# Kernel optimization log

Measured on AMD Instinct MI355X. Metric: run time of the kernel, lower is better.

## Reference

```python
import jax, jax.numpy as jnp
import numpy as np

N = 100000   # nodes of ntype 'gene'
E = 800000   # edges per metapath
D = 256      # input_dim == output_dim
H = 4        # attn heads
C = D // H   # out_channels per head
M = 2        # num metapaths (tail relations = M + 1, last = self)


def _lrelu(x):
    return jnp.where(x >= 0, x, 0.2 * x)


def _segment_softmax(logits, seg, num_segments):
    # logits: [E, H], seg: [E] int targets
    mx = jax.ops.segment_max(logits, seg, num_segments=num_segments)
    mx = jnp.where(jnp.isfinite(mx), mx, 0.0)  # empty segments -> 0
    ex = jnp.exp(logits - mx[seg])
    den = jax.ops.segment_sum(ex, seg, num_segments=num_segments)
    return ex / (den[seg] + 1e-16)


def setup_inputs() -> dict:
    key = jax.random.key(0)
    ks = jax.random.split(key, 10)
    s = 1.0 / np.sqrt(D)
    return {
        "x": jax.random.normal(ks[0], (N, D), dtype=jnp.float32),
        "edge_index0": jax.random.randint(ks[1], (2, E), 0, N, dtype=jnp.int32),
        "edge_index1": jax.random.randint(ks[2], (2, E), 0, N, dtype=jnp.int32),
        "W_l": jax.random.normal(ks[3], (D, D), dtype=jnp.float32) * s,
        "b_l": jnp.zeros((D,), dtype=jnp.float32),
        "W_r": jax.random.normal(ks[4], (D, D), dtype=jnp.float32) * s,
        "b_r": jnp.zeros((D,), dtype=jnp.float32),
        "attn": jax.random.normal(ks[5], (M, H, 2 * C), dtype=jnp.float32) * (1.0 / np.sqrt(2 * C)),
        "rel_attn_l": jax.random.normal(ks[6], (H, C), dtype=jnp.float32) * (1.0 / np.sqrt(C)),
        "rel_attn_r": jax.random.normal(ks[7], (H, C), dtype=jnp.float32) * (1.0 / np.sqrt(C)),
    }


def reference(x, edge_index0, edge_index1, W_l, b_l, W_r, b_r, attn, rel_attn_l, rel_attn_r):
    # projections -> [N, H, C]  (eval mode: dropout/batchnorm off)
    l = (x @ W_l.T + b_l).reshape(N, H, C)
    r = (x @ W_r.T + b_r).reshape(N, H, C)

    # attn split: first C for x_i (target, r-proj), last C for x_j (source, l-proj);
    # leaky_relu is elementwise so the concat+dot separates exactly.
    def agg(edge_index, m_idx):
        src, tgt = edge_index[0], edge_index[1]
        a_i = jnp.einsum('ehc,hc->eh', _lrelu(r[tgt]), attn[m_idx, :, :C])
        a_j = jnp.einsum('ehc,hc->eh', _lrelu(l[src]), attn[m_idx, :, C:])
        alpha = _segment_softmax(a_i + a_j, tgt, N)          # [E, H]
        msg = l[src] * alpha[:, :, None]                      # [E, H, C]
        return jax.ops.segment_sum(msg, tgt, num_segments=N)  # [N, H, C]

    out0 = agg(edge_index0, 0)
    out1 = agg(edge_index1, 1)
    emb = jnp.stack([out0, out1, r], axis=1)                  # [N, M+1, H, C]

    # relation-level beta attention (get_beta_weights)
    alpha_l = jnp.einsum('nhc,hc->nh', r, rel_attn_l)         # [N, H]
    alpha_r = jnp.einsum('nrhc,hc->nrh', emb, rel_attn_r)     # [N, M+1, H]
    beta = jax.nn.softmax(_lrelu(alpha_l[:, None, :] + alpha_r), axis=1)

    h = (emb * beta[..., None]).sum(axis=1).reshape(N, D)
    return jax.nn.relu(h)
```

## Files before the change

kernel.cpp:

```cpp
#include <hip/hip_runtime.h>
#include <hip/hip_bf16.h>
#include <math.h>

#define D_ 256
#define H_ 4
#define C_ 64

typedef __attribute__((ext_vector_type(8))) short short8;
typedef __attribute__((ext_vector_type(4))) float f32x4;

__device__ inline float lrelu(float v) { return v >= 0.f ? v : 0.2f * v; }

__device__ inline unsigned short f2b(float f) {
    unsigned u = __float_as_uint(f);
    u = (u + 0x7FFFu + ((u >> 16) & 1u)) >> 16;
    return (unsigned short)u;
}
__device__ inline float b2f(unsigned short u) {
    return __uint_as_float(((unsigned)u) << 16);
}

#define GLDS(src, dst) __builtin_amdgcn_global_load_lds(                      \
    (const __attribute__((address_space(1))) void*)(src),                     \
    (__attribute__((address_space(3))) void*)(dst), 16, 0, 0)

__global__ __launch_bounds__(256) void convert_w(
    const float* __restrict__ Wl, const float* __restrict__ Wr,
    unsigned short* __restrict__ Wb)
{
    int i4 = blockIdx.x * 256 + threadIdx.x;
    float4 v = (i4 < 16384) ? ((const float4*)Wl)[i4]
                            : ((const float4*)Wr)[i4 - 16384];
    ushort4 u;
    u.x = f2b(v.x); u.y = f2b(v.y); u.z = f2b(v.z); u.w = f2b(v.w);
    ((ushort4*)Wb)[i4] = u;
}

__device__ __forceinline__ void stage_a(const float* __restrict__ x, float* dst,
                                        int bm, int k0, int wv, int lane, int Mrows)
{
#pragma unroll
    for (int p = 0; p < 4; p++) {
        int ci = (p * 4 + wv) * 64 + lane;
        int row = ci >> 3, cc = ci & 7;
        int gr = bm + row; if (gr >= Mrows) gr = Mrows - 1;
        const float* src = x + (size_t)gr * 256 + k0 + ((cc ^ (row & 7)) << 2);
        GLDS(src, (char*)dst + (size_t)(p * 4 + wv) * 1024);
    }
}
__device__ __forceinline__ void stage_b(const unsigned short* __restrict__ W,
                                        unsigned short* dst, int bn, int k0,
                                        int wv, int lane)
{
#pragma unroll
    for (int p = 0; p < 2; p++) {
        int ci = (p * 4 + wv) * 64 + lane;
        int col = ci >> 2, cc = ci & 3;
        const unsigned short* src = W + (size_t)(bn + col) * 256 + k0 +
                                    ((cc ^ (col & 3)) << 3);
        GLDS(src, (char*)dst + (size_t)(p * 4 + wv) * 1024);
    }
}

template <bool RB16>
__global__ __launch_bounds__(256) void gemm_fused(
    const float* __restrict__ x, const unsigned short* __restrict__ Wb,
    const float* __restrict__ b_l, const float* __restrict__ b_r,
    unsigned short* __restrict__ lout, void* __restrict__ rout,
    int Mrows, int nblk)
{
    int hw = blockIdx.x;
    int orig = hw;
    if ((nblk & 7) == 0) {
        int cpx = nblk >> 3;
        orig = (hw & 7) * cpx + (hw >> 3);
    }
    const int sel = (orig & 3) >> 1;
    const int bn = (orig & 1) * 128;
    const int bm = (orig >> 2) * 128;

    __shared__ float As[2][128 * 32];
    __shared__ unsigned short Bs[2][128 * 32];
    const int tid = threadIdx.x;
    const int lane = tid & 63, wv = tid >> 6;
    const int wr = wv >> 1, wc = wv & 1;
    const unsigned short* W = Wb + (size_t)sel * 65536;

    f32x4 acc[4][4];
#pragma unroll
    for (int m = 0; m < 4; m++)
#pragma unroll
        for (int n = 0; n < 4; n++) acc[m][n] = (f32x4)0.f;

    stage_a(x, As[0], bm, 0, wv, lane, Mrows);
    stage_b(W, Bs[0], bn, 0, wv, lane);
    __syncthreads();

    int cur = 0;
#pragma unroll
    for (int t = 0; t < 8; t++) {
        if (t < 7) {
            stage_a(x, As[cur ^ 1], bm, (t + 1) * 32, wv, lane, Mrows);
            stage_b(W, Bs[cur ^ 1], bn, (t + 1) * 32, wv, lane);
        }
        short8 bfr[4];
#pragma unroll
        for (int n = 0; n < 4; n++) {
            int col = wc * 64 + n * 16 + (lane & 15);
            int sc = (lane >> 4) ^ (col & 3);
            bfr[n] = *(const short8*)&Bs[cur][col * 32 + sc * 8];
        }
        short8 afr[4];
#pragma unroll
        for (int m = 0; m < 4; m++) {
            int row = wr * 64 + m * 16 + (lane & 15);
            int c0 = (lane >> 4) * 2;
            const float* ap = &As[cur][row * 32];
            float4 f0 = *(const float4*)&ap[(c0 ^ (row & 7)) << 2];
            float4 f1 = *(const float4*)&ap[((c0 + 1) ^ (row & 7)) << 2];
            union { short8 v; __hip_bfloat162 b2[4]; } u;
            u.b2[0] = __float22bfloat162_rn(make_float2(f0.x, f0.y));
            u.b2[1] = __float22bfloat162_rn(make_float2(f0.z, f0.w));
            u.b2[2] = __float22bfloat162_rn(make_float2(f1.x, f1.y));
            u.b2[3] = __float22bfloat162_rn(make_float2(f1.z, f1.w));
            afr[m] = u.v;
        }
#pragma unroll
        for (int m = 0; m < 4; m++)
#pragma unroll
            for (int n = 0; n < 4; n++)
                acc[m][n] = __builtin_amdgcn_mfma_f32_16x16x32_bf16(
                    afr[m], bfr[n], acc[m][n], 0, 0, 0);
        __syncthreads();
        cur ^= 1;
    }

    const float* bias = sel ? b_r : b_l;
#pragma unroll
    for (int m = 0; m < 4; m++) {
        int grow0 = bm + wr * 64 + m * 16 + (lane >> 4) * 4;
#pragma unroll
        for (int n = 0; n < 4; n++) {
            int gcol = bn + wc * 64 + n * 16 + (lane & 15);
            float bv = bias[gcol];
#pragma unroll
            for (int q = 0; q < 4; q++) {
                int grow = grow0 + q;
                if (grow < Mrows) {
                    float v = acc[m][n][q] + bv;
                    if (sel == 0) {
                        lout[(size_t)grow * 256 + gcol] = f2b(v);
                    } else {
                        if (RB16) ((unsigned short*)rout)[(size_t)grow * 256 + gcol] = f2b(v);
                        else      ((float*)rout)[(size_t)grow * 256 + gcol] = v;
                    }
                }
            }
        }
    }
}

template <bool RB16>
__global__ __launch_bounds__(256) void node_logits(
    const unsigned short* __restrict__ l, const void* __restrict__ rv,
    const float* __restrict__ attn, const float* __restrict__ rel_l,
    const float* __restrict__ rel_r,
    float2* __restrict__ ej2, float* __restrict__ al, float* __restrict__ rd,
    int Nn)
{
    int lane = threadIdx.x & 63;
    int n = blockIdx.x * 4 + (threadIdx.x >> 6);
    if (n >= Nn) return;
    int h = lane >> 4, q = lane & 15;

    ushort4 lv4 = *(const ushort4*)&l[(size_t)n * D_ + lane * 4];
    float rf[4];
    if (RB16) {
        ushort4 ru = ((const ushort4*)rv)[(size_t)n * 64 + lane];
        rf[0] = b2f(ru.x); rf[1] = b2f(ru.y); rf[2] = b2f(ru.z); rf[3] = b2f(ru.w);
    } else {
        float4 rv4 = ((const float4*)rv)[(size_t)n * 64 + lane];
        rf[0] = rv4.x; rf[1] = rv4.y; rf[2] = rv4.z; rf[3] = rv4.w;
    }
    float4 a0 = *(const float4*)&attn[(0 * H_ + h) * 128 + 64 + q * 4];
    float4 a1 = *(const float4*)&attn[(1 * H_ + h) * 128 + 64 + q * 4];
    float4 wl = *(const float4*)&rel_l[h * C_ + q * 4];
    float4 wr = *(const float4*)&rel_r[h * C_ + q * 4];

    float lf[4] = { b2f(lv4.x), b2f(lv4.y), b2f(lv4.z), b2f(lv4.w) };
    float af0[4] = { a0.x, a0.y, a0.z, a0.w };
    float af1[4] = { a1.x, a1.y, a1.z, a1.w };
    float wlf[4] = { wl.x, wl.y, wl.z, wl.w };
    float wrf[4] = { wr.x, wr.y, wr.z, wr.w };

    float v2 = 0.f, v3 = 0.f, v4 = 0.f, v5 = 0.f, v6 = 0.f;
#pragma unroll
    for (int k = 0; k < 4; k++) {
        float ll = lrelu(lf[k]);
        v2 = fmaf(ll, af0[k], v2);
        v3 = fmaf(ll, af1[k], v3);
        v4 = fmaf(rf[k], wlf[k], v4);
        v5 = fmaf(lf[k], wrf[k], v5);
        v6 = fmaf(rf[k], wrf[k], v6);
    }
#pragma unroll
    for (int off = 1; off < 16; off <<= 1) {
        v2 += __shfl_xor(v2, off);
        v3 += __shfl_xor(v3, off);
        v4 += __shfl_xor(v4, off);
        v5 += __shfl_xor(v5, off);
        v6 += __shfl_xor(v6, off);
    }
    if (q == 0) {
        int NH = Nn * H_;
        int nh = n * H_ + h;
        float e0 = __expf(v2), e1 = __expf(v3);
        ej2[nh]      = make_float2(e0, e0 * v5);
        ej2[NH + nh] = make_float2(e1, e1 * v5);
        al[nh] = v4;
        rd[nh] = v6;
    }
}

__global__ __launch_bounds__(256) void edge_hist(
    const int* __restrict__ ei0, const int* __restrict__ ei1,
    int* __restrict__ hist, int E_, int Nn)
{
    int e = blockIdx.x * 256 + threadIdx.x;
    if (e >= E_) return;
    atomicAdd(&hist[ei0[E_ + e]], 1);
    atomicAdd(&hist[Nn + ei1[E_ + e]], 1);
}

__global__ __launch_bounds__(256) void scan_a(
    const int* __restrict__ hist, int* __restrict__ segoff,
    int* __restrict__ bsum, int Nn)
{
    int m = blockIdx.y;
    int gid = blockIdx.x * 256 + threadIdx.x;
    int lane = threadIdx.x & 63, wid = threadIdx.x >> 6;
    int v = (gid < Nn) ? hist[m * Nn + gid] : 0;
    int incl = v;
#pragma unroll
    for (int off = 1; off < 64; off <<= 1) {
        int u = __shfl_up(incl, off);
        if (lane >= off) incl += u;
    }
    __shared__ int ws[4], wo[4];
    if (lane == 63) ws[wid] = incl;
    __syncthreads();
    if (threadIdx.x == 0) {
        int run = 0;
#pragma unroll
        for (int i = 0; i < 4; i++) { wo[i] = run; run += ws[i]; }
        bsum[m * 512 + blockIdx.x] = run;
    }
    __syncthreads();
    if (gid < Nn) segoff[m * Nn + gid] = incl - v + wo[wid];
}

__global__ __launch_bounds__(512) void scan_b(int* __restrict__ bsum, int nb)
{
    int m = blockIdx.x;
    int* b = bsum + m * 512;
    int tid = threadIdx.x, lane = tid & 63, wid = tid >> 6;
    int v = (tid < nb) ? b[tid] : 0;
    int incl = v;
#pragma unroll
    for (int off = 1; off < 64; off <<= 1) {
        int u = __shfl_up(incl, off);
        if (lane >= off) incl += u;
    }
    __shared__ int ws[8], wo[8];
    if (lane == 63) ws[wid] = incl;
    __syncthreads();
    if (tid == 0) {
        int run = 0;
#pragma unroll
        for (int i = 0; i < 8; i++) { wo[i] = run; run += ws[i]; }
    }
    __syncthreads();
    if (tid < nb) b[tid] = incl - v + wo[wid];
}

__global__ __launch_bounds__(256) void edge_scatter(
    const int* __restrict__ ei0, const int* __restrict__ ei1,
    const int* __restrict__ segoff, const int* __restrict__ bsum,
    int* __restrict__ cursor, int* __restrict__ srcs, int E_, int Nn)
{
    int e = blockIdx.x * 256 + threadIdx.x;
    if (e >= E_) return;
    int t0 = ei0[E_ + e];
    int p0 = segoff[t0] + bsum[t0 >> 8] + atomicAdd(&cursor[t0], 1);
    srcs[p0] = ei0[e];
    int t1 = ei1[E_ + e];
    int p1 = segoff[Nn + t1] + bsum[512 + (t1 >> 8)] + atomicAdd(&cursor[Nn + t1], 1);
    srcs[E_ + p1] = ei1[e];
}

template <bool RB16>
__global__ __launch_bounds__(256) void aggregate(
    const int* __restrict__ hist, const int* __restrict__ segoff,
    const int* __restrict__ bsum,
    const int* __restrict__ srcs, const float2* __restrict__ ej2,
    const float* __restrict__ al, const float* __restrict__ rd,
    const void* __restrict__ rv, const unsigned short* __restrict__ l,
    float* __restrict__ out, int Nn, int E_)
{
    int lane = threadIdx.x & 63;
    int t = blockIdx.x * 4 + (threadIdx.x >> 6);
    if (t >= Nn) return;
    int h = lane >> 4;
    int NH = Nn * H_;
    int nh = t * H_ + h;

    float4 rrow;
    if (RB16) {
        ushort4 ru = ((const ushort4*)rv)[(size_t)t * 64 + lane];
        rrow = make_float4(b2f(ru.x), b2f(ru.y), b2f(ru.z), b2f(ru.w));
    } else {
        rrow = ((const float4*)rv)[(size_t)t * 64 + lane];
    }
    float a = al[nh];
    float rdv = rd[nh];

    int beg0 = segoff[t]      + bsum[t >> 8],         deg0 = hist[t];
    int beg1 = segoff[Nn + t] + bsum[512 + (t >> 8)], deg1 = hist[Nn + t];

    float4 acc0 = make_float4(0.f, 0.f, 0.f, 0.f);
    float4 acc1 = make_float4(0.f, 0.f, 0.f, 0.f);
    float den0 = 0.f, pn0 = 0.f, den1 = 0.f, pn1 = 0.f;

#pragma unroll 4
    for (int j = 0; j < deg0; j++) {
        int s = srcs[beg0 + j];
        float2 v = ej2[(size_t)s * H_ + h];
        den0 += v.x; pn0 += v.y;
        ushort4 lv = *(const ushort4*)&l[(size_t)s * D_ + lane * 4];
        acc0.x = fmaf(b2f(lv.x), v.x, acc0.x);
        acc0.y = fmaf(b2f(lv.y), v.x, acc0.y);
        acc0.z = fmaf(b2f(lv.z), v.x, acc0.z);
        acc0.w = fmaf(b2f(lv.w), v.x, acc0.w);
    }
    const float2* ep1 = ej2 + NH;
#pragma unroll 4
    for (int j = 0; j < deg1; j++) {
        int s = srcs[E_ + beg1 + j];
        float2 v = ep1[(size_t)s * H_ + h];
        den1 += v.x; pn1 += v.y;
        ushort4 lv = *(const ushort4*)&l[(size_t)s * D_ + lane * 4];
        acc1.x = fmaf(b2f(lv.x), v.x, acc1.x);
        acc1.y = fmaf(b2f(lv.y), v.x, acc1.y);
        acc1.z = fmaf(b2f(lv.z), v.x, acc1.z);
        acc1.w = fmaf(b2f(lv.w), v.x, acc1.w);
    }

    float b0 = lrelu(a + pn0 / (den0 + 1e-16f));
    float b1 = lrelu(a + pn1 / (den1 + 1e-16f));
    float b2 = lrelu(a + rdv);
    float mm = fmaxf(b0, fmaxf(b1, b2));
    float e0 = __expf(b0 - mm), e1 = __expf(b1 - mm), e2 = __expf(b2 - mm);
    float inv = 1.f / (e0 + e1 + e2);
    float wm0 = e0 * inv / (den0 + 1e-16f);
    float wm1 = e1 * inv / (den1 + 1e-16f);
    float b2v = e2 * inv;

    float4 o;
    o.x = fmaxf(fmaf(wm0, acc0.x, fmaf(wm1, acc1.x, b2v * rrow.x)), 0.f);
    o.y = fmaxf(fmaf(wm0, acc0.y, fmaf(wm1, acc1.y, b2v * rrow.y)), 0.f);
    o.z = fmaxf(fmaf(wm0, acc0.z, fmaf(wm1, acc1.z, b2v * rrow.z)), 0.f);
    o.w = fmaxf(fmaf(wm0, acc0.w, fmaf(wm1, acc1.w, b2v * rrow.w)), 0.f);
    *(float4*)&out[(size_t)t * D_ + lane * 4] = o;
}

extern "C" void kernel_launch(void* const* d_in, const int* in_sizes, int n_in,
                              void* d_out, int out_size, void* d_ws, size_t ws_size,
                              hipStream_t stream) {
    const float* x     = (const float*)d_in[0];
    const int*   ei0   = (const int*)d_in[1];
    const int*   ei1   = (const int*)d_in[2];
    const float* W_l   = (const float*)d_in[3];
    const float* b_l   = (const float*)d_in[4];
    const float* W_r   = (const float*)d_in[5];
    const float* b_r   = (const float*)d_in[6];
    const float* attn  = (const float*)d_in[7];
    const float* rel_l = (const float*)d_in[8];
    const float* rel_r = (const float*)d_in[9];
    float* out = (float*)d_out;

    const int Nn = in_sizes[0] / D_;
    const int E_ = in_sizes[1] / 2;
    const size_t ND = (size_t)Nn * D_;
    const int NH = Nn * H_;

    char* base = (char*)d_ws;
    unsigned short* l = (unsigned short*)base;      size_t off = ND * 2;
    float2* ej2  = (float2*)(base + off); off += (size_t)2 * NH * 8;
    float* al    = (float*)(base + off);  off += (size_t)NH * 4;
    float* rd    = (float*)(base + off);  off += (size_t)NH * 4;
    int* hist    = (int*)(base + off);    off += (size_t)2 * Nn * 4;
    int* cursor  = (int*)(base + off);    off += (size_t)2 * Nn * 4;
    int* segoff  = (int*)(base + off);    off += (size_t)2 * Nn * 4;
    int* bsum    = (int*)(base + off);    off += (size_t)1024 * 4;
    int* srcs    = (int*)(base + off);    off += (size_t)2 * E_ * 4;
    unsigned short* Wb = (unsigned short*)(base + off); off += (size_t)2 * 65536 * 2;
    unsigned short* rb = (unsigned short*)(base + off);
    const bool rb16 = (ws_size >= off + ND * 2);
    void* r_any = rb16 ? (void*)rb : (void*)out;

    hipMemsetAsync(hist, 0, (size_t)4 * Nn * 4, stream);

    convert_w<<<128, 256, 0, stream>>>(W_l, W_r, Wb);

    int rowTiles = (Nn + 127) / 128;
    int nblk = 4 * rowTiles;
    if (rb16)
        gemm_fused<true ><<<nblk, 256, 0, stream>>>(x, Wb, b_l, b_r, l, r_any, Nn, nblk);
    else
        gemm_fused<false><<<nblk, 256, 0, stream>>>(x, Wb, b_l, b_r, l, r_any, Nn, nblk);

    if (rb16)
        node_logits<true ><<<(Nn + 3) / 4, 256, 0, stream>>>(
            l, r_any, attn, rel_l, rel_r, ej2, al, rd, Nn);
    else
        node_logits<false><<<(Nn + 3) / 4, 256, 0, stream>>>(
            l, r_any, attn, rel_l, rel_r, ej2, al, rd, Nn);

    int eb = (E_ + 255) / 256;
    int nb = (Nn + 255) / 256;
    edge_hist<<<eb, 256, 0, stream>>>(ei0, ei1, hist, E_, Nn);
    scan_a<<<dim3(nb, 2), 256, 0, stream>>>(hist, segoff, bsum, Nn);
    scan_b<<<2, 512, 0, stream>>>(bsum, nb);
    edge_scatter<<<eb, 256, 0, stream>>>(ei0, ei1, segoff, bsum, cursor, srcs, E_, Nn);

    if (rb16)
        aggregate<true ><<<(Nn + 3) / 4, 256, 0, stream>>>(
            hist, segoff, bsum, srcs, ej2, al, rd, r_any, l, out, Nn, E_);
    else
        aggregate<false><<<(Nn + 3) / 4, 256, 0, stream>>>(
            hist, segoff, bsum, srcs, ej2, al, rd, r_any, l, out, Nn, E_);
}
```

Measured before the change: 446.7 us.

## Fuse node logits into GEMM epilogue and split aggregation across metapath waves

```diff
diff --git a/kernel.cpp b/kernel.cpp
--- a/kernel.cpp
+++ b/kernel.cpp
@@ -66,7 +66,10 @@
 __global__ __launch_bounds__(256) void gemm_fused(
     const float* __restrict__ x, const unsigned short* __restrict__ Wb,
     const float* __restrict__ b_l, const float* __restrict__ b_r,
+    const float* __restrict__ attn, const float* __restrict__ rel_l,
+    const float* __restrict__ rel_r,
     unsigned short* __restrict__ lout, void* __restrict__ rout,
+    float2* __restrict__ ej2, float* __restrict__ al, float* __restrict__ rd,
     int Mrows, int nblk)
 {
     int hw = blockIdx.x;
@@ -136,89 +139,71 @@
     }
 
     const float* bias = sel ? b_r : b_l;
+    const int NH = Mrows * H_;
+    const int h = (bn >> 6) + wc;
+    float bv[4], w0[4], w1[4], w2[4];
+    int gcol[4];
+#pragma unroll
+    for (int n = 0; n < 4; n++) {
+        int c = n * 16 + (lane & 15);
+        gcol[n] = bn + wc * 64 + c - (wc * 64 + c) + wc * 64 + c;
+        gcol[n] = bn + wc * 64 + c;
+        bv[n] = bias[gcol[n]];
+        if (sel == 0) {
+            w0[n] = attn[(0 * H_ + h) * 128 + 64 + c];
+            w1[n] = attn[(1 * H_ + h) * 128 + 64 + c];
+            w2[n] = rel_r[h * C_ + c];
+        } else {
+            w0[n] = rel_l[h * C_ + c];
+            w1[n] = rel_r[h * C_ + c];
+        }
+    }
 #pragma unroll
     for (int m = 0; m < 4; m++) {
-        int grow0 = bm + wr * 64 + m * 16 + (lane >> 4) * 4;
-#pragma unroll
-        for (int n = 0; n < 4; n++) {
-            int gcol = bn + wc * 64 + n * 16 + (lane & 15);
-            float bv = bias[gcol];
-#pragma unroll
-            for (int q = 0; q < 4; q++) {
-                int grow = grow0 + q;
-                if (grow < Mrows) {
-                    float v = acc[m][n][q] + bv;
+#pragma unroll
+        for (int q = 0; q < 4; q++) {
+            int grow = bm + wr * 64 + m * 16 + (lane >> 4) * 4 + q;
+            bool ok = grow < Mrows;
+            float p0 = 0.f, p1 = 0.f, p2 = 0.f;
+#pragma unroll
+            for (int n = 0; n < 4; n++) {
+                float v = acc[m][n][q] + bv[n];
+                if (ok) {
                     if (sel == 0) {
-                        lout[(size_t)grow * 256 + gcol] = f2b(v);
+                        lout[(size_t)grow * 256 + gcol[n]] = f2b(v);
                     } else {
-                        if (RB16) ((unsigned short*)rout)[(size_t)grow * 256 + gcol] = f2b(v);
-                        else      ((float*)rout)[(size_t)grow * 256 + gcol] = v;
+                        if (RB16) ((unsigned short*)rout)[(size_t)grow * 256 + gcol[n]] = f2b(v);
+                        else      ((float*)rout)[(size_t)grow * 256 + gcol[n]] = v;
                     }
                 }
+                if (sel == 0) {
+                    float lr = lrelu(v);
+                    p0 = fmaf(lr, w0[n], p0);
+                    p1 = fmaf(lr, w1[n], p1);
+                    p2 = fmaf(v, w2[n], p2);
+                } else {
+                    p0 = fmaf(v, w0[n], p0);
+                    p1 = fmaf(v, w1[n], p1);
+                }
             }
-        }
-    }
-}
-
-template <bool RB16>
-__global__ __launch_bounds__(256) void node_logits(
-    const unsigned short* __restrict__ l, const void* __restrict__ rv,
-    const float* __restrict__ attn, const float* __restrict__ rel_l,
-    const float* __restrict__ rel_r,
-    float2* __restrict__ ej2, float* __restrict__ al, float* __restrict__ rd,
-    int Nn)
-{
-    int lane = threadIdx.x & 63;
-    int n = blockIdx.x * 4 + (threadIdx.x >> 6);
-    if (n >= Nn) return;
-    int h = lane >> 4, q = lane & 15;
-
-    ushort4 lv4 = *(const ushort4*)&l[(size_t)n * D_ + lane * 4];
-    float rf[4];
-    if (RB16) {
-        ushort4 ru = ((const ushort4*)rv)[(size_t)n * 64 + lane];
-        rf[0] = b2f(ru.x); rf[1] = b2f(ru.y); rf[2] = b2f(ru.z); rf[3] = b2f(ru.w);
-    } else {
-        float4 rv4 = ((const float4*)rv)[(size_t)n * 64 + lane];
-        rf[0] = rv4.x; rf[1] = rv4.y; rf[2] = rv4.z; rf[3] = rv4.w;
-    }
-    float4 a0 = *(const float4*)&attn[(0 * H_ + h) * 128 + 64 + q * 4];
-    float4 a1 = *(const float4*)&attn[(1 * H_ + h) * 128 + 64 + q * 4];
-    float4 wl = *(const float4*)&rel_l[h * C_ + q * 4];
-    float4 wr = *(const float4*)&rel_r[h * C_ + q * 4];
-
-    float lf[4] = { b2f(lv4.x), b2f(lv4.y), b2f(lv4.z), b2f(lv4.w) };
-    float af0[4] = { a0.x, a0.y, a0.z, a0.w };
-    float af1[4] = { a1.x, a1.y, a1.z, a1.w };
-    float wlf[4] = { wl.x, wl.y, wl.z, wl.w };
-    float wrf[4] = { wr.x, wr.y, wr.z, wr.w };
-
-    float v2 = 0.f, v3 = 0.f, v4 = 0.f, v5 = 0.f, v6 = 0.f;
-#pragma unroll
-    for (int k = 0; k < 4; k++) {
-        float ll = lrelu(lf[k]);
-        v2 = fmaf(ll, af0[k], v2);
-        v3 = fmaf(ll, af1[k], v3);
-        v4 = fmaf(rf[k], wlf[k], v4);
-        v5 = fmaf(lf[k], wrf[k], v5);
-        v6 = fmaf(rf[k], wrf[k], v6);
-    }
-#pragma unroll
-    for (int off = 1; off < 16; off <<= 1) {
-        v2 += __shfl_xor(v2, off);
-        v3 += __shfl_xor(v3, off);
-        v4 += __shfl_xor(v4, off);
-        v5 += __shfl_xor(v5, off);
-        v6 += __shfl_xor(v6, off);
-    }
-    if (q == 0) {
-        int NH = Nn * H_;
-        int nh = n * H_ + h;
-        float e0 = __expf(v2), e1 = __expf(v3);
-        ej2[nh]      = make_float2(e0, e0 * v5);
-        ej2[NH + nh] = make_float2(e1, e1 * v5);
-        al[nh] = v4;
-        rd[nh] = v6;
+#pragma unroll
+            for (int off = 1; off < 16; off <<= 1) {
+                p0 += __shfl_xor(p0, off);
+                p1 += __shfl_xor(p1, off);
+                if (sel == 0) p2 += __shfl_xor(p2, off);
+            }
+            if (ok && (lane & 15) == 0) {
+                int nh = grow * H_ + h;
+                if (sel == 0) {
+                    float e0 = __expf(p0), e1 = __expf(p1);
+                    ej2[nh]      = make_float2(e0, e0 * p2);
+                    ej2[NH + nh] = make_float2(e1, e1 * p2);
+                } else {
+                    al[nh] = p0;
+                    rd[nh] = p1;
+                }
+            }
+        }
     }
 }
 
@@ -307,69 +292,74 @@
     const void* __restrict__ rv, const unsigned short* __restrict__ l,
     float* __restrict__ out, int Nn, int E_)
 {
+    __shared__ float4 accS[2][64];
+    __shared__ float2 dpS[2][64];
     int lane = threadIdx.x & 63;
-    int t = blockIdx.x * 4 + (threadIdx.x >> 6);
-    if (t >= Nn) return;
+    int wid = threadIdx.x >> 6;
+    int pair = wid >> 1, mp = wid & 1;
+    int t = blockIdx.x * 2 + pair;
+    bool active = t < Nn;
     int h = lane >> 4;
     int NH = Nn * H_;
     int nh = t * H_ + h;
 
-    float4 rrow;
-    if (RB16) {
-        ushort4 ru = ((const ushort4*)rv)[(size_t)t * 64 + lane];
-        rrow = make_float4(b2f(ru.x), b2f(ru.y), b2f(ru.z), b2f(ru.w));
-    } else {
-        rrow = ((const float4*)rv)[(size_t)t * 64 + lane];
-    }
-    float a = al[nh];
-    float rdv = rd[nh];
-
-    int beg0 = segoff[t]      + bsum[t >> 8],         deg0 = hist[t];
-    int beg1 = segoff[Nn + t] + bsum[512 + (t >> 8)], deg1 = hist[Nn + t];
-
-    float4 acc0 = make_float4(0.f, 0.f, 0.f, 0.f);
-    float4 acc1 = make_float4(0.f, 0.f, 0.f, 0.f);
-    float den0 = 0.f, pn0 = 0.f, den1 = 0.f, pn1 = 0.f;
-
+    float4 rrow = make_float4(0.f, 0.f, 0.f, 0.f);
+    float a = 0.f, rdv = 0.f;
+    if (active && mp == 0) {
+        if (RB16) {
+            ushort4 ru = ((const ushort4*)rv)[(size_t)t * 64 + lane];
+            rrow = make_float4(b2f(ru.x), b2f(ru.y), b2f(ru.z), b2f(ru.w));
+        } else {
+            rrow = ((const float4*)rv)[(size_t)t * 64 + lane];
+        }
+        a = al[nh];
+        rdv = rd[nh];
+    }
+
+    float4 acc = make_float4(0.f, 0.f, 0.f, 0.f);
+    float den = 0.f, pn = 0.f;
+    if (active) {
+        int beg = segoff[mp * Nn + t] + bsum[mp * 512 + (t >> 8)];
+        int deg = hist[mp * Nn + t];
+        const int* sp = srcs + (size_t)mp * E_;
+        const float2* ep = ej2 + (size_t)mp * NH;
 #pragma unroll 4
-    for (int j = 0; j < deg0; j++) {
-        int s = srcs[beg0 + j];
-        float2 v = ej2[(size_t)s * H_ + h];
-        den0 += v.x; pn0 += v.y;
-        ushort4 lv = *(const ushort4*)&l[(size_t)s * D_ + lane * 4];
-        acc0.x = fmaf(b2f(lv.x), v.x, acc0.x);
-        acc0.y = fmaf(b2f(lv.y), v.x, acc0.y);
-        acc0.z = fmaf(b2f(lv.z), v.x, acc0.z);
-        acc0.w = fmaf(b2f(lv.w), v.x, acc0.w);
-    }
-    const float2* ep1 = ej2 + NH;
-#pragma unroll 4
-    for (int j = 0; j < deg1; j++) {
-        int s = srcs[E_ + beg1 + j];
-        float2 v = ep1[(size_t)s * H_ + h];
-        den1 += v.x; pn1 += v.y;
-        ushort4 lv = *(const ushort4*)&l[(size_t)s * D_ + lane * 4];
-        acc1.x = fmaf(b2f(lv.x), v.x, acc1.x);
-        acc1.y = fmaf(b2f(lv.y), v.x, acc1.y);
-        acc1.z = fmaf(b2f(lv.z), v.x, acc1.z);
-        acc1.w = fmaf(b2f(lv.w), v.x, acc1.w);
-    }
-
-    float b0 = lrelu(a + pn0 / (den0 + 1e-16f));
-    float b1 = lrelu(a + pn1 / (den1 + 1e-16f));
+        for (int j = 0; j < deg; j++) {
+            int s = sp[beg + j];
+            float2 v = ep[(size_t)s * H_ + h];
+            den += v.x; pn += v.y;
+            ushort4 lv = *(const ushort4*)&l[(size_t)s * D_ + lane * 4];
+            acc.x = fmaf(b2f(lv.x), v.x, acc.x);
+            acc.y = fmaf(b2f(lv.y), v.x, acc.y);
+            acc.z = fmaf(b2f(lv.z), v.x, acc.z);
+            acc.w = fmaf(b2f(lv.w), v.x, acc.w);
+        }
+    }
+    if (mp == 1) {
+        accS[pair][lane] = acc;
+        dpS[pair][lane] = make_float2(den, pn);
+    }
+    __syncthreads();
+    if (mp == 1 || !active) return;
+
+    float4 acc1 = accS[pair][lane];
+    float2 dp1 = dpS[pair][lane];
+
+    float b0 = lrelu(a + pn / (den + 1e-16f));
+    float b1 = lrelu(a + dp1.y / (dp1.x + 1e-16f));
     float b2 = lrelu(a + rdv);
     float mm = fmaxf(b0, fmaxf(b1, b2));
     float e0 = __expf(b0 - mm), e1 = __expf(b1 - mm), e2 = __expf(b2 - mm);
     float inv = 1.f / (e0 + e1 + e2);
-    float wm0 = e0 * inv / (den0 + 1e-16f);
-    float wm1 = e1 * inv / (den1 + 1e-16f);
+    float wm0 = e0 * inv / (den + 1e-16f);
+    float wm1 = e1 * inv / (dp1.x + 1e-16f);
     float b2v = e2 * inv;
 
     float4 o;
-    o.x = fmaxf(fmaf(wm0, acc0.x, fmaf(wm1, acc1.x, b2v * rrow.x)), 0.f);
-    o.y = fmaxf(fmaf(wm0, acc0.y, fmaf(wm1, acc1.y, b2v * rrow.y)), 0.f);
-    o.z = fmaxf(fmaf(wm0, acc0.z, fmaf(wm1, acc1.z, b2v * rrow.z)), 0.f);
-    o.w = fmaxf(fmaf(wm0, acc0.w, fmaf(wm1, acc1.w, b2v * rrow.w)), 0.f);
+    o.x = fmaxf(fmaf(wm0, acc.x, fmaf(wm1, acc1.x, b2v * rrow.x)), 0.f);
+    o.y = fmaxf(fmaf(wm0, acc.y, fmaf(wm1, acc1.y, b2v * rrow.y)), 0.f);
+    o.z = fmaxf(fmaf(wm0, acc.z, fmaf(wm1, acc1.z, b2v * rrow.z)), 0.f);
+    o.w = fmaxf(fmaf(wm0, acc.w, fmaf(wm1, acc1.w, b2v * rrow.w)), 0.f);
     *(float4*)&out[(size_t)t * D_ + lane * 4] = o;
 }
 
@@ -415,16 +405,11 @@
     int rowTiles = (Nn + 127) / 128;
     int nblk = 4 * rowTiles;
     if (rb16)
-        gemm_fused<true ><<<nblk, 256, 0, stream>>>(x, Wb, b_l, b_r, l, r_any, Nn, nblk);
+        gemm_fused<true ><<<nblk, 256, 0, stream>>>(
+            x, Wb, b_l, b_r, attn, rel_l, rel_r, l, r_any, ej2, al, rd, Nn, nblk);
     else
-        gemm_fused<false><<<nblk, 256, 0, stream>>>(x, Wb, b_l, b_r, l, r_any, Nn, nblk);
-
-    if (rb16)
-        node_logits<true ><<<(Nn + 3) / 4, 256, 0, stream>>>(
-            l, r_any, attn, rel_l, rel_r, ej2, al, rd, Nn);
-    else
-        node_logits<false><<<(Nn + 3) / 4, 256, 0, stream>>>(
-            l, r_any, attn, rel_l, rel_r, ej2, al, rd, Nn);
+        gemm_fused<false><<<nblk, 256, 0, stream>>>(
+            x, Wb, b_l, b_r, attn, rel_l, rel_r, l, r_any, ej2, al, rd, Nn, nblk);
 
     int eb = (E_ + 255) / 256;
     int nb = (Nn + 255) / 256;
@@ -434,9 +419,9 @@
     edge_scatter<<<eb, 256, 0, stream>>>(ei0, ei1, segoff, bsum, cursor, srcs, E_, Nn);
 
     if (rb16)
-        aggregate<true ><<<(Nn + 3) / 4, 256, 0, stream>>>(
+        aggregate<true ><<<(Nn + 1) / 2, 256, 0, stream>>>(
             hist, segoff, bsum, srcs, ej2, al, rd, r_any, l, out, Nn, E_);
     else
-        aggregate<false><<<(Nn + 3) / 4, 256, 0, stream>>>(
+        aggregate<false><<<(Nn + 1) / 2, 256, 0, stream>>>(
             hist, segoff, bsum, srcs, ej2, al, rd, r_any, l, out, Nn, E_);
 }
```

Measured after the change: 441.2 us. No clear change (-1.2%).
